# Optimization experiments

Hardware: AMD Instinct MI355X
Metric: run time of the kernel (lower is better)

Reference implementation:

```python
import jax, jax.numpy as jnp
import numpy as np

UPDATE_RATE = 0.5

def _perception_filters():
    # Fixed per-channel 3x3 stencils: identity, sobel_x, sobel_y, laplacian.
    ident = np.array([[0, 0, 0], [0, 1, 0], [0, 0, 0]], np.float32)
    sobel_x = np.array([[-1, 0, 1], [-2, 0, 2], [-1, 0, 1]], np.float32)
    sobel_y = sobel_x.T
    lap = np.array([[1, 2, 1], [2, -12, 2], [1, 2, 1]], np.float32)
    # HWIO with I=1, O=4 -> grouped (depthwise) conv with feature_group_count=4,
    # matching tf.nn.conv2d semantics for a (3,3,1,4) filter on 4-channel input.
    return np.stack([ident, sobel_x, sobel_y, lap], axis=-1)[:, :, None, :]


def setup_inputs() -> dict:
    key = jax.random.key(0)
    k_in, k_rand, k_w1, k_b1, k_w2 = jax.random.split(key, 5)
    B, H, W, C, HID = 64, 512, 512, 4, 6
    return {
        "inputs": jax.random.normal(k_in, (B, H, W, C), dtype=jnp.float32),
        "rand_vals": jax.random.uniform(k_rand, (B, H, W, 1), dtype=jnp.float32),
        "w1_kernel": jax.random.normal(k_w1, (C, HID), dtype=jnp.float32) * 0.3,
        "w1_bias": jax.random.normal(k_b1, (HID,), dtype=jnp.float32) * 0.1,
        "w2_kernel": jax.random.normal(k_w2, (HID, C), dtype=jnp.float32) * 0.3,
    }


def reference(inputs, rand_vals, w1_kernel, w1_bias, w2_kernel):
    filt = jnp.asarray(_perception_filters())  # (3,3,1,4)
    # circular_padding: toroidal pad by 1 on H and W (square grid assumed).
    x = jnp.pad(inputs, ((0, 0), (1, 1), (1, 1), (0, 0)), mode="wrap")
    # Depthwise 3x3 stencil conv (channel i gets kernel i), VALID -> (B,H,W,4).
    percep = jax.lax.conv_general_dilated(
        x, filt, window_strides=(1, 1), padding="VALID",
        dimension_numbers=("NHWC", "HWIO", "NHWC"), feature_group_count=4)
    # 1x1 conv 4->6 with bias, relu, then 1x1 conv 6->4 without bias.
    h = jax.nn.relu(jnp.einsum("bhwc,cd->bhwd", percep, w1_kernel) + w1_bias)
    dx = jnp.einsum("bhwd,dc->bhwc", h, w2_kernel)
    # Stochastic update mask: floor(U(0,1) + update_rate) in {0,1}.
    update_mask = jnp.floor(rand_vals + UPDATE_RATE)
    return inputs + dx * update_mask
```

## Files before the change

kernel.cpp:

```cpp
#include <hip/hip_runtime.h>


constexpr int H = 512, W = 512, C = 4, HIDN = 6, R = 16;
constexpr int NXCD = 8;

typedef float f32x4 __attribute__((ext_vector_type(4)));

__device__ __forceinline__ f32x4 ld4(const float* p) {
    return *reinterpret_cast<const f32x4*>(p);
}

__global__ __launch_bounds__(256) void ca_kernel(
    const float* __restrict__ x,
    const float* __restrict__ rnd,
    const float* __restrict__ w1,
    const float* __restrict__ b1,
    const float* __restrict__ w2,
    float* __restrict__ out)
{
    const int nblk  = (int)gridDim.x;
    const int chunk = nblk / NXCD;
    const int bid   = (int)blockIdx.x;
    const int swz   = (bid & (NXCD - 1)) * chunk + (bid >> 3);

    const int t = swz * (int)blockDim.x + (int)threadIdx.x;
    const int w     = t & (W - 1);
    const int strip = t >> 9;
    const int h0    = (strip & (H / R - 1)) * R;
    const int b     = strip / (H / R);

    const int wm = (w == 0) ? (W - 1) : (w - 1);
    const int wp = (w == W - 1) ? 0 : (w + 1);

    float w1r[C * HIDN], b1r[HIDN], w2r[HIDN * C];
    #pragma unroll
    for (int i = 0; i < C * HIDN; ++i) w1r[i] = w1[i];
    #pragma unroll
    for (int i = 0; i < HIDN; ++i) b1r[i] = b1[i];
    #pragma unroll
    for (int i = 0; i < HIDN * C; ++i) w2r[i] = w2[i];

    const float* xb = x   + (size_t)b * H * W * C;
    const float* rb = rnd + (size_t)b * H * W;
    float*       ob = out + (size_t)b * H * W * C;

    f32x4 a0, a1, a2, c0, c1, c2, d0, d1, d2;
    {
        const int hm = (h0 == 0) ? (H - 1) : (h0 - 1);
        a0 = ld4(xb + ((hm * W + wm) << 2));
        a1 = ld4(xb + ((hm * W + w ) << 2));
        a2 = ld4(xb + ((hm * W + wp) << 2));
        c0 = ld4(xb + ((h0 * W + wm) << 2));
        c1 = ld4(xb + ((h0 * W + w ) << 2));
        c2 = ld4(xb + ((h0 * W + wp) << 2));
        const int h1 = h0 + 1;
        d0 = ld4(xb + ((h1 * W + wm) << 2));
        d1 = ld4(xb + ((h1 * W + w ) << 2));
        d2 = ld4(xb + ((h1 * W + wp) << 2));
    }

    #pragma unroll
    for (int r = 0; r < R; ++r) {
        const int h = h0 + r;

        const float p0 = c1.x;
        const float p1 = (a2.y - a0.y) + 2.f * (c2.y - c0.y)
                       + (d2.y - d0.y);
        const float p2 = (d0.z - a0.z) + 2.f * (d1.z - a1.z)
                       + (d2.z - a2.z);
        const float p3 = a0.w + 2.f * a1.w + a2.w
                       + 2.f * c0.w - 12.f * c1.w + 2.f * c2.w
                       + d0.w + 2.f * d1.w + d2.w;

        float hid[HIDN];
        #pragma unroll
        for (int j = 0; j < HIDN; ++j) {
            float v = p0 * w1r[j] + p1 * w1r[HIDN + j] + p2 * w1r[2 * HIDN + j]
                    + p3 * w1r[3 * HIDN + j] + b1r[j];
            hid[j] = v > 0.f ? v : 0.f;
        }
        float dx0 = 0.f, dx1 = 0.f, dx2 = 0.f, dx3 = 0.f;
        #pragma unroll
        for (int j = 0; j < HIDN; ++j) {
            dx0 += hid[j] * w2r[j * 4 + 0];
            dx1 += hid[j] * w2r[j * 4 + 1];
            dx2 += hid[j] * w2r[j * 4 + 2];
            dx3 += hid[j] * w2r[j * 4 + 3];
        }

        const float rv = __builtin_nontemporal_load(rb + h * W + w);
        const float mask = floorf(rv + 0.5f);

        f32x4 o;
        o.x = c1.x + dx0 * mask;
        o.y = c1.y + dx1 * mask;
        o.z = c1.z + dx2 * mask;
        o.w = c1.w + dx3 * mask;
        __builtin_nontemporal_store(o, reinterpret_cast<f32x4*>(ob + ((h * W + w) << 2)));

        a0 = c0; a1 = c1; a2 = c2;
        c0 = d0; c1 = d1; c2 = d2;
        if (r < R - 1) {
            int hn = h + 2;
            if (hn >= H) hn -= H;
            d0 = ld4(xb + ((hn * W + wm) << 2));
            d1 = ld4(xb + ((hn * W + w ) << 2));
            d2 = ld4(xb + ((hn * W + wp) << 2));
        }
    }
}

extern "C" void kernel_launch(void* const* d_in, const int* in_sizes, int n_in,
                              void* d_out, int out_size, void* d_ws, size_t ws_size,
                              hipStream_t stream) {
    const float* x   = (const float*)d_in[0];
    const float* rnd = (const float*)d_in[1];
    const float* w1  = (const float*)d_in[2];
    const float* b1  = (const float*)d_in[3];
    const float* w2  = (const float*)d_in[4];
    float* out = (float*)d_out;

    const int B = in_sizes[0] / (H * W * C);
    const int total_threads = B * (H / R) * W;
    dim3 grid(total_threads / 256), block(256);
    hipLaunchKernelGGL(ca_kernel, grid, block, 0, stream, x, rnd, w1, b1, w2, out);
}
```

Baseline: 514.7 us.

## Prefetch stencil rows two ahead with row-reduced partial sums and shorter strips

The strip per thread shrinks from 16 to 8 rows. A two-slot register ring prefetches input rows two rows ahead, and each loaded row is collapsed at once into small partial sums (sobel and laplacian row terms plus the centre value), which cuts the live registers and the per-row arithmetic. The random-mask value is prefetched one row ahead. Nontemporal loads and stores are replaced with ordinary ones, and launch bounds now request higher occupancy. The aim is to hide memory latency in a bandwidth-bound stencil. The cost is more halo rows re-read per output row because the strips are shorter, and possible cache pollution from the plain stores.

```diff
diff --git a/kernel.cpp b/kernel.cpp
--- a/kernel.cpp
+++ b/kernel.cpp
@@ -1,16 +1,27 @@
 #include <hip/hip_runtime.h>
 
 
-constexpr int H = 512, W = 512, C = 4, HIDN = 6, R = 16;
+constexpr int H = 512, W = 512, C = 4, HIDN = 6, R = 8;
 constexpr int NXCD = 8;
 
 typedef float f32x4 __attribute__((ext_vector_type(4)));
+
+struct RowSum { float t, u, v; f32x4 ctr; };
 
 __device__ __forceinline__ f32x4 ld4(const float* p) {
     return *reinterpret_cast<const f32x4*>(p);
 }
 
-__global__ __launch_bounds__(256) void ca_kernel(
+__device__ __forceinline__ RowSum reduce_row(f32x4 l, f32x4 c, f32x4 r) {
+    RowSum s;
+    s.t = r.y - l.y;
+    s.u = __builtin_fmaf(2.f, c.z, l.z + r.z);
+    s.v = __builtin_fmaf(2.f, c.w, l.w + r.w);
+    s.ctr = c;
+    return s;
+}
+
+__global__ __launch_bounds__(256, 8) void ca_kernel(
     const float* __restrict__ x,
     const float* __restrict__ rnd,
     const float* __restrict__ w1,
@@ -27,10 +38,11 @@
     const int w     = t & (W - 1);
     const int strip = t >> 9;
     const int h0    = (strip & (H / R - 1)) * R;
-    const int b     = strip / (H / R);
+    const int b     = strip >> 6;
 
     const int wm = (w == 0) ? (W - 1) : (w - 1);
     const int wp = (w == W - 1) ? 0 : (w + 1);
+    const int om = wm << 2, oc = w << 2, op = wp << 2;
 
     float w1r[C * HIDN], b1r[HIDN], w2r[HIDN * C];
     #pragma unroll
@@ -44,33 +56,32 @@
     const float* rb = rnd + (size_t)b * H * W;
     float*       ob = out + (size_t)b * H * W * C;
 
-    f32x4 a0, a1, a2, c0, c1, c2, d0, d1, d2;
+    RowSum sa, sc, sd;
+    f32x4 bl[2], bc[2], br[2];
     {
         const int hm = (h0 == 0) ? (H - 1) : (h0 - 1);
-        a0 = ld4(xb + ((hm * W + wm) << 2));
-        a1 = ld4(xb + ((hm * W + w ) << 2));
-        a2 = ld4(xb + ((hm * W + wp) << 2));
-        c0 = ld4(xb + ((h0 * W + wm) << 2));
-        c1 = ld4(xb + ((h0 * W + w ) << 2));
-        c2 = ld4(xb + ((h0 * W + wp) << 2));
-        const int h1 = h0 + 1;
-        d0 = ld4(xb + ((h1 * W + wm) << 2));
-        d1 = ld4(xb + ((h1 * W + w ) << 2));
-        d2 = ld4(xb + ((h1 * W + wp) << 2));
+        const float* r0 = xb + (size_t)hm * (W * C);
+        const float* r1 = xb + (size_t)h0 * (W * C);
+        const float* r2 = xb + (size_t)(h0 + 1) * (W * C);
+        const float* r3 = xb + (size_t)(h0 + 2) * (W * C);
+        const float* r4 = xb + (size_t)(h0 + 3) * (W * C);
+        sa = reduce_row(ld4(r0 + om), ld4(r0 + oc), ld4(r0 + op));
+        sc = reduce_row(ld4(r1 + om), ld4(r1 + oc), ld4(r1 + op));
+        sd = reduce_row(ld4(r2 + om), ld4(r2 + oc), ld4(r2 + op));
+        bl[0] = ld4(r3 + om); bc[0] = ld4(r3 + oc); br[0] = ld4(r3 + op);
+        bl[1] = ld4(r4 + om); bc[1] = ld4(r4 + oc); br[1] = ld4(r4 + op);
     }
+
+    float rv_next = rb[h0 * W + w];
 
     #pragma unroll
     for (int r = 0; r < R; ++r) {
         const int h = h0 + r;
 
-        const float p0 = c1.x;
-        const float p1 = (a2.y - a0.y) + 2.f * (c2.y - c0.y)
-                       + (d2.y - d0.y);
-        const float p2 = (d0.z - a0.z) + 2.f * (d1.z - a1.z)
-                       + (d2.z - a2.z);
-        const float p3 = a0.w + 2.f * a1.w + a2.w
-                       + 2.f * c0.w - 12.f * c1.w + 2.f * c2.w
-                       + d0.w + 2.f * d1.w + d2.w;
+        const float p0 = sc.ctr.x;
+        const float p1 = (sa.t + sd.t) + 2.f * sc.t;
+        const float p2 = sd.u - sa.u;
+        const float p3 = (sa.v + sd.v) + 2.f * sc.v - 16.f * sc.ctr.w;
 
         float hid[HIDN];
         #pragma unroll
@@ -88,24 +99,28 @@
             dx3 += hid[j] * w2r[j * 4 + 3];
         }
 
-        const float rv = __builtin_nontemporal_load(rb + h * W + w);
-        const float mask = floorf(rv + 0.5f);
+        const float mask = floorf(rv_next + 0.5f);
+        if (r < R - 1) rv_next = rb[(h + 1) * W + w];
 
         f32x4 o;
-        o.x = c1.x + dx0 * mask;
-        o.y = c1.y + dx1 * mask;
-        o.z = c1.z + dx2 * mask;
-        o.w = c1.w + dx3 * mask;
-        __builtin_nontemporal_store(o, reinterpret_cast<f32x4*>(ob + ((h * W + w) << 2)));
+        o.x = sc.ctr.x + dx0 * mask;
+        o.y = sc.ctr.y + dx1 * mask;
+        o.z = sc.ctr.z + dx2 * mask;
+        o.w = sc.ctr.w + dx3 * mask;
+        *reinterpret_cast<f32x4*>(ob + ((h * W + w) << 2)) = o;
 
-        a0 = c0; a1 = c1; a2 = c2;
-        c0 = d0; c1 = d1; c2 = d2;
         if (r < R - 1) {
-            int hn = h + 2;
-            if (hn >= H) hn -= H;
-            d0 = ld4(xb + ((hn * W + wm) << 2));
-            d1 = ld4(xb + ((hn * W + w ) << 2));
-            d2 = ld4(xb + ((hn * W + wp) << 2));
+            sa = sc; sc = sd;
+            const int ib = r & 1;
+            sd = reduce_row(bl[ib], bc[ib], br[ib]);
+            if (r <= R - 4) {
+                int hn = h + 4;
+                if (hn >= H) hn -= H;
+                const float* rp = xb + (size_t)hn * (W * C);
+                bl[ib] = ld4(rp + om);
+                bc[ib] = ld4(rp + oc);
+                br[ib] = ld4(rp + op);
+            }
         }
     }
 }
```

Result: slower. 902.4 us (+75.3%).

## Replace per-thread row-strip sliding window with one thread per pixel

Applied to the files above, without the earlier changes.

Drops the 16-row sliding-window loop so each thread computes a single output pixel and loads all nine neighbours directly. This raises parallelism and removes the serial dependency along the strip. In exchange each input row is loaded three times instead of about once, leaving the extra reuse to caches. It also replaces the nontemporal loads and stores with ordinary ones.

```diff
diff --git a/kernel.cpp b/kernel.cpp
--- a/kernel.cpp
+++ b/kernel.cpp
@@ -1,7 +1,7 @@
 #include <hip/hip_runtime.h>
 
 
-constexpr int H = 512, W = 512, C = 4, HIDN = 6, R = 16;
+constexpr int H = 512, W = 512, C = 4, HIDN = 6;
 constexpr int NXCD = 8;
 
 typedef float f32x4 __attribute__((ext_vector_type(4)));
@@ -24,13 +24,25 @@
     const int swz   = (bid & (NXCD - 1)) * chunk + (bid >> 3);
 
     const int t = swz * (int)blockDim.x + (int)threadIdx.x;
-    const int w     = t & (W - 1);
-    const int strip = t >> 9;
-    const int h0    = (strip & (H / R - 1)) * R;
-    const int b     = strip / (H / R);
+    const int w = t & (W - 1);
+    const int h = (t >> 9) & (H - 1);
+    const int b = t >> 18;
 
     const int wm = (w == 0) ? (W - 1) : (w - 1);
     const int wp = (w == W - 1) ? 0 : (w + 1);
+    const int hm = (h == 0) ? (H - 1) : (h - 1);
+    const int hp = (h == H - 1) ? 0 : (h + 1);
+    const int om = wm << 2, oc = w << 2, op = wp << 2;
+
+    const float* xb = x + (size_t)b * (H * W * C);
+    const float* rA = xb + (size_t)hm * (W * C);
+    const float* rC = xb + (size_t)h  * (W * C);
+    const float* rD = xb + (size_t)hp * (W * C);
+
+    const f32x4 a0 = ld4(rA + om), a1 = ld4(rA + oc), a2 = ld4(rA + op);
+    const f32x4 c0 = ld4(rC + om), c1 = ld4(rC + oc), c2 = ld4(rC + op);
+    const f32x4 d0 = ld4(rD + om), d1 = ld4(rD + oc), d2 = ld4(rD + op);
+    const float rv = rnd[(size_t)b * (H * W) + h * W + w];
 
     float w1r[C * HIDN], b1r[HIDN], w2r[HIDN * C];
     #pragma unroll
@@ -40,74 +52,39 @@
     #pragma unroll
     for (int i = 0; i < HIDN * C; ++i) w2r[i] = w2[i];
 
-    const float* xb = x   + (size_t)b * H * W * C;
-    const float* rb = rnd + (size_t)b * H * W;
-    float*       ob = out + (size_t)b * H * W * C;
+    const float p0 = c1.x;
+    const float p1 = (a2.y - a0.y) + 2.f * (c2.y - c0.y)
+                   + (d2.y - d0.y);
+    const float p2 = (d0.z - a0.z) + 2.f * (d1.z - a1.z)
+                   + (d2.z - a2.z);
+    const float p3 = a0.w + 2.f * a1.w + a2.w
+                   + 2.f * c0.w - 12.f * c1.w + 2.f * c2.w
+                   + d0.w + 2.f * d1.w + d2.w;
 
-    f32x4 a0, a1, a2, c0, c1, c2, d0, d1, d2;
-    {
-        const int hm = (h0 == 0) ? (H - 1) : (h0 - 1);
-        a0 = ld4(xb + ((hm * W + wm) << 2));
-        a1 = ld4(xb + ((hm * W + w ) << 2));
-        a2 = ld4(xb + ((hm * W + wp) << 2));
-        c0 = ld4(xb + ((h0 * W + wm) << 2));
-        c1 = ld4(xb + ((h0 * W + w ) << 2));
-        c2 = ld4(xb + ((h0 * W + wp) << 2));
-        const int h1 = h0 + 1;
-        d0 = ld4(xb + ((h1 * W + wm) << 2));
-        d1 = ld4(xb + ((h1 * W + w ) << 2));
-        d2 = ld4(xb + ((h1 * W + wp) << 2));
+    float hid[HIDN];
+    #pragma unroll
+    for (int j = 0; j < HIDN; ++j) {
+        float v = p0 * w1r[j] + p1 * w1r[HIDN + j] + p2 * w1r[2 * HIDN + j]
+                + p3 * w1r[3 * HIDN + j] + b1r[j];
+        hid[j] = v > 0.f ? v : 0.f;
+    }
+    float dx0 = 0.f, dx1 = 0.f, dx2 = 0.f, dx3 = 0.f;
+    #pragma unroll
+    for (int j = 0; j < HIDN; ++j) {
+        dx0 += hid[j] * w2r[j * 4 + 0];
+        dx1 += hid[j] * w2r[j * 4 + 1];
+        dx2 += hid[j] * w2r[j * 4 + 2];
+        dx3 += hid[j] * w2r[j * 4 + 3];
     }
 
-    #pragma unroll
-    for (int r = 0; r < R; ++r) {
-        const int h = h0 + r;
+    const float mask = floorf(rv + 0.5f);
 
-        const float p0 = c1.x;
-        const float p1 = (a2.y - a0.y) + 2.f * (c2.y - c0.y)
-                       + (d2.y - d0.y);
-        const float p2 = (d0.z - a0.z) + 2.f * (d1.z - a1.z)
-                       + (d2.z - a2.z);
-        const float p3 = a0.w + 2.f * a1.w + a2.w
-                       + 2.f * c0.w - 12.f * c1.w + 2.f * c2.w
-                       + d0.w + 2.f * d1.w + d2.w;
-
-        float hid[HIDN];
-        #pragma unroll
-        for (int j = 0; j < HIDN; ++j) {
-            float v = p0 * w1r[j] + p1 * w1r[HIDN + j] + p2 * w1r[2 * HIDN + j]
-                    + p3 * w1r[3 * HIDN + j] + b1r[j];
-            hid[j] = v > 0.f ? v : 0.f;
-        }
-        float dx0 = 0.f, dx1 = 0.f, dx2 = 0.f, dx3 = 0.f;
-        #pragma unroll
-        for (int j = 0; j < HIDN; ++j) {
-            dx0 += hid[j] * w2r[j * 4 + 0];
-            dx1 += hid[j] * w2r[j * 4 + 1];
-            dx2 += hid[j] * w2r[j * 4 + 2];
-            dx3 += hid[j] * w2r[j * 4 + 3];
-        }
-
-        const float rv = __builtin_nontemporal_load(rb + h * W + w);
-        const float mask = floorf(rv + 0.5f);
-
-        f32x4 o;
-        o.x = c1.x + dx0 * mask;
-        o.y = c1.y + dx1 * mask;
-        o.z = c1.z + dx2 * mask;
-        o.w = c1.w + dx3 * mask;
-        __builtin_nontemporal_store(o, reinterpret_cast<f32x4*>(ob + ((h * W + w) << 2)));
-
-        a0 = c0; a1 = c1; a2 = c2;
-        c0 = d0; c1 = d1; c2 = d2;
-        if (r < R - 1) {
-            int hn = h + 2;
-            if (hn >= H) hn -= H;
-            d0 = ld4(xb + ((hn * W + wm) << 2));
-            d1 = ld4(xb + ((hn * W + w ) << 2));
-            d2 = ld4(xb + ((hn * W + wp) << 2));
-        }
-    }
+    f32x4 o;
+    o.x = c1.x + dx0 * mask;
+    o.y = c1.y + dx1 * mask;
+    o.z = c1.z + dx2 * mask;
+    o.w = c1.w + dx3 * mask;
+    *reinterpret_cast<f32x4*>(out + (size_t)b * (H * W * C) + ((h * W + w) << 2)) = o;
 }
 
 extern "C" void kernel_launch(void* const* d_in, const int* in_sizes, int n_in,
@@ -121,7 +98,7 @@
     float* out = (float*)d_out;
 
     const int B = in_sizes[0] / (H * W * C);
-    const int total_threads = B * (H / R) * W;
-    dim3 grid(total_threads / 256), block(256);
+    const long long total_threads = (long long)B * H * W;
+    dim3 grid((unsigned)(total_threads / 256)), block(256);
     hipLaunchKernelGGL(ca_kernel, grid, block, 0, stream, x, rnd, w1, b1, w2, out);
 }
```

Measured after the change: 500.6 us. -2.7%, faster.
